# Kernel optimization log

Hardware: AMD Instinct MI355X
Metric: run time of the kernel (lower is better)

## Reference

```python
import jax, jax.numpy as jnp
import numpy as np

N, G, E = 100000, 32768, 1000000
F, H = 64, 64


def _mlp(x, w1, b1, w2, b2):
    # Linear -> SiLU -> Linear (matches nn.Sequential in the torch module)
    return jax.nn.silu(x @ w1 + b1) @ w2 + b2


def setup_inputs() -> dict:
    key = jax.random.key(0)
    ks = jax.random.split(key, 24)

    def lin(k, fan_in, fan_out):
        s = 1.0 / np.sqrt(fan_in)
        kw, kb = jax.random.split(k)
        w = jax.random.uniform(kw, (fan_in, fan_out), jnp.float32, -s, s)
        b = jax.random.uniform(kb, (fan_out,), jnp.float32, -s, s)
        return w, b

    node_w1, node_b1 = lin(ks[0], F, H)
    node_w2, node_b2 = lin(ks[1], H, H)
    edge_w1, edge_b1 = lin(ks[2], 6, H)
    edge_w2, edge_b2 = lin(ks[3], H, H)
    msg_w1, msg_b1 = lin(ks[4], 2 * H, H)
    msg_w2, msg_b2 = lin(ks[5], H, H)
    upd_w1, upd_b1 = lin(ks[6], H, H)
    upd_w2, upd_b2 = lin(ks[7], H, H)

    return {
        "node_features": jax.random.normal(ks[8], (N, F), jnp.float32),
        "node_pos": jax.random.normal(ks[9], (N, 3), jnp.float32),
        "grid_pos": jax.random.normal(ks[10], (G, 3), jnp.float32),
        "orientations": jax.random.normal(ks[11], (N, 3, 3), jnp.float32),
        "edge_index": jnp.stack([
            jax.random.randint(ks[12], (E,), 0, N),
            jax.random.randint(ks[13], (E,), 0, G),
        ]),
        "node_w1": node_w1, "node_b1": node_b1, "node_w2": node_w2, "node_b2": node_b2,
        "edge_w1": edge_w1, "edge_b1": edge_b1, "edge_w2": edge_w2, "edge_b2": edge_b2,
        "msg_w1": msg_w1, "msg_b1": msg_b1, "msg_w2": msg_w2, "msg_b2": msg_b2,
        "upd_w1": upd_w1, "upd_b1": upd_b1, "upd_w2": upd_w2, "upd_b2": upd_b2,
    }


def reference(node_features, node_pos, grid_pos, orientations, edge_index,
              node_w1, node_b1, node_w2, node_b2,
              edge_w1, edge_b1, edge_w2, edge_b2,
              msg_w1, msg_b1, msg_w2, msg_b2,
              upd_w1, upd_b1, upd_w2, upd_b2):
    source, target = edge_index[0], edge_index[1]
    num_grid = grid_pos.shape[0]

    # node MLP
    h_node = _mlp(node_features, node_w1, node_b1, node_w2, node_b2)  # [N,H]

    # per-edge message with orientation-aware projection
    pos_s = node_pos[source]                 # [E,3]
    rel = grid_pos[target] - pos_s           # [E,3]
    # bmm(rel[:,None,:], R[source]).squeeze(1) == einsum ei,eij->ej
    trel = jnp.einsum("ei,eij->ej", rel, orientations[source])
    edge_attr = jnp.concatenate([pos_s, trel], axis=-1)        # [E,6]
    e_feat = _mlp(edge_attr, edge_w1, edge_b1, edge_w2, edge_b2)
    msg_in = jnp.concatenate([h_node[source], e_feat], axis=-1)  # [E,2H]
    messages = _mlp(msg_in, msg_w1, msg_b1, msg_w2, msg_b2)      # [E,H]

    # scatter-mean into grid buckets (mask out-of-range targets)
    valid = (target >= 0) & (target < num_grid)
    idx = jnp.where(valid, target, 0)
    msg_masked = jnp.where(valid[:, None], messages, 0.0)
    sums = jax.ops.segment_sum(msg_masked, idx, num_segments=num_grid)
    cnts = jax.ops.segment_sum(valid.astype(jnp.float32), idx, num_segments=num_grid)
    grid_feat = sums / jnp.maximum(cnts, 1.0)[:, None]

    return _mlp(grid_feat, upd_w1, upd_b1, upd_w2, upd_b2)  # [G,H]
```

## Files before the change

### kernel.cpp

```cpp
#include <hip/hip_runtime.h>
#include <hip/hip_bf16.h>
#include <cstdint>

typedef __attribute__((ext_vector_type(8))) short short8;
typedef __attribute__((ext_vector_type(4))) float f32x4;
typedef unsigned short u16;

__device__ __forceinline__ float b2f(u16 u) {
  union { unsigned int i; float f; } v; v.i = ((unsigned int)u) << 16; return v.f;
}
__device__ __forceinline__ u16 f2b(float f) {
  __hip_bfloat16 h = __float2bfloat16(f);
  union { __hip_bfloat16 h; u16 u; } v; v.h = h; return v.u;
}
__device__ __forceinline__ float silu_f(float x) {
  return x * __builtin_amdgcn_rcpf(1.0f + __expf(-x));
}

__device__ __forceinline__ float loadF(const void* p, long i, int isf32) {
  if (isf32) return ((const float*)p)[i];
  return b2f(((const u16*)p)[i]);
}

__device__ __forceinline__ int sniffbit(u16 u) {
  unsigned e = (u >> 7) & 0xffu;
  return (e >= 0xC0u || (e < 0x40u && (u & 0x7fffu) != 0)) ? 1 : 0;
}

struct Ptrs { const void* p[20]; int n[20]; };

#define FW_EW1 0
#define FW_UW1 384
#define FW_UW2 4480
#define FW_UB1 8576
#define FW_UB2 8640
#define FW_EB1 8704
#define FW_EB2 8768
#define FW_MB1 8832
#define FW_MB2 8896
#define FW_TOTAL 8960

#define IMG_EW2 0
#define IMG_MW1 4608
#define IMG_MW2 13312
#define IMG_TOTAL 17920

#define PREP_BLOCKS 105
#define HIST_BLOCKS 1024

__global__ __launch_bounds__(256) void hist_detect_k(
    Ptrs a, const int* __restrict__ eidx, int* __restrict__ cnt8,
    int* __restrict__ flags, long E, int G)
{
  const int t = threadIdx.x;
  const int b = blockIdx.x;
  if (b < HIST_BLOCKS) {
    int* cs = cnt8 + (size_t)(b & 7) * G;
    long i = (long)b * 256 + t;
    const long stride = (long)HIST_BLOCKS * 256;
    for (; i < E; i += stride) {
      int tg = eidx[E + i];
      if (tg >= 0 && tg < G) atomicAdd(&cs[tg], 1);
    }
    return;
  }
  int j = b - HIST_BLOCKS;
  const u16* q = (const u16*)a.p[j];
  int n = a.n[j];
  int m = n < 4096 ? n : 4096;
  int cnt = 0;
  for (int i = t; i < m; i += 256) cnt += sniffbit(q[i]);
  __shared__ int tot;
  if (t == 0) tot = 0;
  __syncthreads();
  if (cnt) atomicAdd(&tot, cnt);
  __syncthreads();
  if (t == 0) flags[j] = (tot >= 2) ? 1 : 0;
}

__global__ __launch_bounds__(256) void scan_prep_node_k(
    Ptrs a, const int* __restrict__ flags,
    const int* __restrict__ cnt8, int* __restrict__ cursor8,
    int* __restrict__ bsum,
    u16* __restrict__ img, float* __restrict__ fw,
    u16* __restrict__ hout, int nrows, int G, int NB2)
{
  const int t = threadIdx.x;
  const int b = blockIdx.x;

  if (b < NB2) {
    __shared__ int sd[256];
    const long tot = 8L * G;
    long j0 = (long)b * 1024 + (long)t * 4;
    int v[4];
#pragma unroll
    for (int k = 0; k < 4; ++k) {
      long j = j0 + k;
      v[k] = (j < tot) ? cnt8[(size_t)(j & 7) * G + (j >> 3)] : 0;
    }
    int local = v[0] + v[1] + v[2] + v[3];
    sd[t] = local;
    __syncthreads();
    for (int off = 1; off < 256; off <<= 1) {
      int x2 = (t >= off) ? sd[t - off] : 0;
      __syncthreads();
      sd[t] += x2;
      __syncthreads();
    }
    int p = sd[t] - local;
#pragma unroll
    for (int k = 0; k < 4; ++k) {
      long j = j0 + k;
      if (j < tot) cursor8[(size_t)(j & 7) * G + (j >> 3)] = p;
      p += v[k];
    }
    if (t == 255) bsum[b] = sd[255];
    return;
  }

  if (b < NB2 + PREP_BLOCKS) {
    int i = (b - NB2) * 256 + t;
    if (i < IMG_TOTAL) {
      const void* bp; int fl; long si; bool real;
      if (i < IMG_MW1) { int nn = i / 72, k = i % 72; bp = a.p[10]; fl = flags[10]; real = k < 64; si = (long)k * 64 + nn; }
      else if (i < IMG_MW2) { int t2 = i - IMG_MW1; int nn = t2 / 136, k = t2 % 136; bp = a.p[12]; fl = flags[12]; real = k < 128; si = (long)k * 64 + nn; }
      else { int t2 = i - IMG_MW2; int nn = t2 / 72, k = t2 % 72; bp = a.p[14]; fl = flags[14]; real = k < 64; si = (long)k * 64 + nn; }
      u16 val = 0;
      if (real) val = f2b(loadF(bp, si, fl));
      img[i] = val;
    } else if (i < IMG_TOTAL + FW_TOTAL) {
      int j = i - IMG_TOTAL;
      const void* bp; int fl; long si;
      if (j < 384)        { bp = a.p[8];  fl = flags[8];  si = j; }
      else if (j < 4480)  { bp = a.p[16]; fl = flags[16]; si = j - 384; }
      else if (j < 8576)  { bp = a.p[18]; fl = flags[18]; si = j - 4480; }
      else {
        int bb = j - 8576; int seg = bb >> 6; si = bb & 63;
        switch (seg) {
          case 0: bp = a.p[17]; fl = flags[17]; break;
          case 1: bp = a.p[19]; fl = flags[19]; break;
          case 2: bp = a.p[9];  fl = flags[9];  break;
          case 3: bp = a.p[11]; fl = flags[11]; break;
          case 4: bp = a.p[13]; fl = flags[13]; break;
          default: bp = a.p[15]; fl = flags[15]; break;
        }
      }
      fw[j] = loadF(bp, si, fl);
    }
    return;
  }

  __shared__ float xs[64][68];
  __shared__ float w1s[64][68];
  __shared__ float w2s[64][68];
  __shared__ float b1s[64];
  __shared__ float b2s[64];
  const void* x = a.p[0];
  const int xf = flags[0], f1 = flags[4], fb1 = flags[5], f2 = flags[6], fb2 = flags[7];
  const long rbase = (long)(b - NB2 - PREP_BLOCKS) * 64;
  for (int i = t; i < 4096; i += 256) {
    int k = i >> 6, cc = i & 63;
    w1s[k][cc] = loadF(a.p[4], i, f1);
    w2s[k][cc] = loadF(a.p[6], i, f2);
  }
  if (t < 64) { b1s[t] = loadF(a.p[5], t, fb1); b2s[t] = loadF(a.p[7], t, fb2); }
  {
    int row = t >> 2, ch = t & 3;
    long rg = rbase + row;
    if (rg < nrows) {
      if (xf) {
        const float* xp = (const float*)x + rg * 64 + ch * 16;
#pragma unroll
        for (int m = 0; m < 16; ++m) xs[row][ch * 16 + m] = xp[m];
      } else {
        const u16* xp = (const u16*)x + rg * 64 + ch * 16;
#pragma unroll
        for (int m = 0; m < 16; ++m) xs[row][ch * 16 + m] = b2f(xp[m]);
      }
    } else {
#pragma unroll
      for (int m = 0; m < 16; ++m) xs[row][ch * 16 + m] = 0.f;
    }
  }
  __syncthreads();
  const int r0 = (t >> 4) * 4, c0 = (t & 15) * 4;
  float acc[4][4];
#pragma unroll
  for (int i = 0; i < 4; ++i)
#pragma unroll
    for (int j = 0; j < 4; ++j) acc[i][j] = b1s[c0 + j];
  for (int k = 0; k < 64; ++k) {
    float w0 = w1s[k][c0], w1v = w1s[k][c0 + 1], w2v = w1s[k][c0 + 2], w3v = w1s[k][c0 + 3];
#pragma unroll
    for (int i = 0; i < 4; ++i) {
      float av = xs[r0 + i][k];
      acc[i][0] = fmaf(av, w0, acc[i][0]);
      acc[i][1] = fmaf(av, w1v, acc[i][1]);
      acc[i][2] = fmaf(av, w2v, acc[i][2]);
      acc[i][3] = fmaf(av, w3v, acc[i][3]);
    }
  }
  __syncthreads();
#pragma unroll
  for (int i = 0; i < 4; ++i)
#pragma unroll
    for (int j = 0; j < 4; ++j) xs[r0 + i][c0 + j] = silu_f(acc[i][j]);
  __syncthreads();
  float acc2[4][4];
#pragma unroll
  for (int i = 0; i < 4; ++i)
#pragma unroll
    for (int j = 0; j < 4; ++j) acc2[i][j] = b2s[c0 + j];
  for (int k = 0; k < 64; ++k) {
    float w0 = w2s[k][c0], w1v = w2s[k][c0 + 1], w2v = w2s[k][c0 + 2], w3v = w2s[k][c0 + 3];
#pragma unroll
    for (int i = 0; i < 4; ++i) {
      float av = xs[r0 + i][k];
      acc2[i][0] = fmaf(av, w0, acc2[i][0]);
      acc2[i][1] = fmaf(av, w1v, acc2[i][1]);
      acc2[i][2] = fmaf(av, w2v, acc2[i][2]);
      acc2[i][3] = fmaf(av, w3v, acc2[i][3]);
    }
  }
#pragma unroll
  for (int i = 0; i < 4; ++i) {
    long rg = rbase + r0 + i;
    if (rg < nrows) {
#pragma unroll
      for (int j = 0; j < 4; ++j) hout[rg * 64 + c0 + j] = f2b(acc2[i][j]);
    }
  }
}

__global__ __launch_bounds__(256) void scat_k(const int* __restrict__ eidx,
                                              int* __restrict__ cursor8,
                                              const int* __restrict__ bsum,
                                              unsigned int* __restrict__ pkS,
                                              int* __restrict__ evp,
                                              long E, int G, int NB2) {
  __shared__ int bo[256];
  const int t = threadIdx.x;
  int v = (t < NB2) ? bsum[t] : 0;
  bo[t] = v;
  __syncthreads();
  for (int off = 1; off < 256; off <<= 1) {
    int x2 = (t >= off) ? bo[t - off] : 0;
    __syncthreads();
    bo[t] += x2;
    __syncthreads();
  }
  if (blockIdx.x == 0 && t == 0) *evp = bo[NB2 - 1];
  int excl = bo[t] - v;
  __syncthreads();
  bo[t] = excl;
  __syncthreads();
  const int c = blockIdx.x & 7;
  int* cur = cursor8 + (size_t)c * G;
  long i = (long)blockIdx.x * 256 + t;
  const long stride = (long)gridDim.x * 256;
  for (; i < E; i += stride) {
    int tg = eidx[E + i];
    if (tg >= 0 && tg < G) {
      int s = eidx[i];
      long j = ((long)tg << 3) | c;
      int p = atomicAdd(&cur[tg], 1) + bo[j >> 10];
      __builtin_nontemporal_store((unsigned int)s | ((unsigned int)tg << 17), pkS + p);
    }
  }
}

#define ETILES 4

__global__ __launch_bounds__(256, 5) void edge_kernel(
    const void* node_pos, const void* grid_pos, const void* orient,
    const unsigned int* __restrict__ pkS, const int* __restrict__ evp,
    const u16* __restrict__ h_node, const u16* __restrict__ img,
    const float* __restrict__ fw, const int* __restrict__ flags,
    float* __restrict__ sums, int G)
{
  __shared__ __align__(16) u16 pool[4][3328];
  __shared__ float eaf[64][6];
  __shared__ float w1e[6][64];
  __shared__ float biasE[4][64];
  __shared__ int tgt_s[64];

  const int t = threadIdx.x;
  const int pf = flags[1], gf = flags[2], of = flags[3];
  const int Ev = *evp;
  for (int i = t; i < 384; i += 256) w1e[i / 64][i % 64] = fw[FW_EW1 + i];
  { int seg = t >> 6, cc = t & 63; biasE[seg][cc] = fw[FW_EB1 + seg * 64 + cc]; }
  __syncthreads();

  const int lane = t & 63, w = t >> 6;
  const int q = lane >> 4, c = lane & 15;
  const int m0 = w * 16;
  u16 (* __restrict__ ef1w)[72] = (u16 (*)[72])&pool[w][0];
  u16 (* __restrict__ hAw)[136] = (u16 (*)[136])&pool[w][1152];
  float (* __restrict__ msgfw)[66] = (float (*)[66])&pool[w][1152];
  const u16* wE2 = img + IMG_EW2;
  const u16* wM1 = img + IMG_MW1;
  const u16* wM2 = img + IMG_MW2;
  const f32x4 z = {0.f, 0.f, 0.f, 0.f};

  const long blockBase = (long)blockIdx.x * (ETILES * 64);

  unsigned int pkt[ETILES];
#pragma unroll
  for (int tn = 0; tn < ETILES; ++tn) {
    long eg = blockBase + (long)tn * 64 + m0 + lane;
    pkt[tn] = (lane < 16 && eg < Ev) ? pkS[eg] : 0u;
  }

  float gps[3], ggp[3], gor[9];
  int gtg = -1;
  short8 hv0, hv1;

  auto prefetch = [&](int tn) {
    long tb = blockBase + (long)tn * 64;
    unsigned int pk = pkt[tn];
    int gs = (int)(pk & 0x1FFFFu);
    gtg = (int)(pk >> 17);
    if (tb + m0 + lane >= Ev) { gs = 0; gtg = -1; }
    if (lane < 16) {
      int tgc = (gtg >= 0) ? gtg : 0;
#pragma unroll
      for (int i = 0; i < 3; ++i) gps[i] = loadF(node_pos, (long)gs * 3 + i, pf);
#pragma unroll
      for (int i = 0; i < 3; ++i) ggp[i] = loadF(grid_pos, (long)tgc * 3 + i, gf);
#pragma unroll
      for (int i = 0; i < 9; ++i) gor[i] = loadF(orient, (long)gs * 9 + i, of);
    }
    unsigned int pk2 = (unsigned int)__shfl((int)pkt[tn], lane >> 2);
    int ss = ((tb + m0 + (lane >> 2)) < Ev) ? (int)(pk2 & 0x1FFFFu) : 0;
    const u16* hp = h_node + (long)ss * 64 + (lane & 3) * 16;
    hv0 = *(const short8*)hp;
    hv1 = *(const short8*)(hp + 8);
  };

  prefetch(0);

#pragma unroll
  for (int tile = 0; tile < ETILES; ++tile) {
    long base = blockBase + (long)tile * 64;
    if (base >= Ev) break;

    if (lane < 16) {
      tgt_s[m0 + lane] = gtg;
      float rel[3], tr[3];
#pragma unroll
      for (int i = 0; i < 3; ++i) rel[i] = ggp[i] - gps[i];
#pragma unroll
      for (int j = 0; j < 3; ++j) tr[j] = 0.f;
#pragma unroll
      for (int i = 0; i < 3; ++i)
#pragma unroll
        for (int j = 0; j < 3; ++j) tr[j] = fmaf(rel[i], gor[i * 3 + j], tr[j]);
      eaf[m0 + lane][0] = gps[0]; eaf[m0 + lane][1] = gps[1]; eaf[m0 + lane][2] = gps[2];
      eaf[m0 + lane][3] = tr[0]; eaf[m0 + lane][4] = tr[1]; eaf[m0 + lane][5] = tr[2];
    }
    {
      int er = lane >> 2, ch = lane & 3;
      *(short8*)&hAw[er][ch * 16] = hv0;
      *(short8*)&hAw[er][ch * 16 + 8] = hv1;
    }
    __syncthreads();

    {
      int e = lane >> 2, c0 = (lane & 3) * 16;
      int eb = m0 + e;
      float a0 = eaf[eb][0], a1 = eaf[eb][1], a2 = eaf[eb][2];
      float a3 = eaf[eb][3], a4 = eaf[eb][4], a5 = eaf[eb][5];
      __align__(16) u16 tmp[16];
#pragma unroll
      for (int j = 0; j < 16; ++j) {
        int cc = c0 + j;
        float acc = biasE[0][cc];
        acc = fmaf(a0, w1e[0][cc], acc);
        acc = fmaf(a1, w1e[1][cc], acc);
        acc = fmaf(a2, w1e[2][cc], acc);
        acc = fmaf(a3, w1e[3][cc], acc);
        acc = fmaf(a4, w1e[4][cc], acc);
        acc = fmaf(a5, w1e[5][cc], acc);
        tmp[j] = f2b(silu_f(acc));
      }
      *(short8*)&ef1w[e][c0] = *(const short8*)tmp;
      *(short8*)&ef1w[e][c0 + 8] = *(const short8*)(tmp + 8);
    }
    __builtin_amdgcn_wave_barrier();
    {
      short8 a0 = *(const short8*)&ef1w[c][q * 8];
      short8 a1 = *(const short8*)&ef1w[c][32 + q * 8];
#pragma unroll
      for (int nt = 0; nt < 4; ++nt) {
        short8 b0 = *(const short8*)&wE2[(nt * 16 + c) * 72 + q * 8];
        short8 b1v = *(const short8*)&wE2[(nt * 16 + c) * 72 + 32 + q * 8];
        f32x4 acc = __builtin_amdgcn_mfma_f32_16x16x32_bf16(a0, b0, z, 0, 0, 0);
        acc = __builtin_amdgcn_mfma_f32_16x16x32_bf16(a1, b1v, acc, 0, 0, 0);
#pragma unroll
        for (int r = 0; r < 4; ++r) {
          int row = q * 4 + r, col = nt * 16 + c;
          hAw[row][64 + col] = f2b(acc[r] + biasE[1][col]);
        }
      }
    }
    __builtin_amdgcn_wave_barrier();
    {
      short8 a0 = *(const short8*)&hAw[c][q * 8];
      short8 a1 = *(const short8*)&hAw[c][32 + q * 8];
      short8 a2 = *(const short8*)&hAw[c][64 + q * 8];
      short8 a3 = *(const short8*)&hAw[c][96 + q * 8];
#pragma unroll
      for (int nt = 0; nt < 4; ++nt) {
        const u16* wp = &wM1[(nt * 16 + c) * 136];
        f32x4 acc = __builtin_amdgcn_mfma_f32_16x16x32_bf16(a0, *(const short8*)(wp + q * 8), z, 0, 0, 0);
        acc = __builtin_amdgcn_mfma_f32_16x16x32_bf16(a1, *(const short8*)(wp + 32 + q * 8), acc, 0, 0, 0);
        acc = __builtin_amdgcn_mfma_f32_16x16x32_bf16(a2, *(const short8*)(wp + 64 + q * 8), acc, 0, 0, 0);
        acc = __builtin_amdgcn_mfma_f32_16x16x32_bf16(a3, *(const short8*)(wp + 96 + q * 8), acc, 0, 0, 0);
#pragma unroll
        for (int r = 0; r < 4; ++r) {
          int row = q * 4 + r, col = nt * 16 + c;
          ef1w[row][col] = f2b(silu_f(acc[r] + biasE[2][col]));
        }
      }
    }
    __builtin_amdgcn_wave_barrier();
    {
      short8 a0 = *(const short8*)&ef1w[c][q * 8];
      short8 a1 = *(const short8*)&ef1w[c][32 + q * 8];
      __builtin_amdgcn_wave_barrier();
#pragma unroll
      for (int nt = 0; nt < 4; ++nt) {
        short8 b0 = *(const short8*)&wM2[(nt * 16 + c) * 72 + q * 8];
        short8 b1v = *(const short8*)&wM2[(nt * 16 + c) * 72 + 32 + q * 8];
        f32x4 acc = __builtin_amdgcn_mfma_f32_16x16x32_bf16(a0, b0, z, 0, 0, 0);
        acc = __builtin_amdgcn_mfma_f32_16x16x32_bf16(a1, b1v, acc, 0, 0, 0);
#pragma unroll
        for (int r = 0; r < 4; ++r) {
          int row = q * 4 + r, col = nt * 16 + c;
          msgfw[row][col] = acc[r] + biasE[3][col];
        }
      }
    }
    __builtin_amdgcn_wave_barrier();

    __builtin_amdgcn_sched_barrier(0);
    if (tile + 1 < ETILES && base + 64 < Ev) prefetch(tile + 1);

    {
      int col = lane;
      int cur = tgt_s[m0];
      float run = msgfw[0][col];
      bool lopen = (m0 == 0) ? true : (tgt_s[m0 - 1] == cur);
#pragma unroll
      for (int r2 = 1; r2 < 16; ++r2) {
        int tg = tgt_s[m0 + r2];
        float v = msgfw[r2][col];
        if (tg == cur) {
          run += v;
        } else {
          if (cur >= 0) {
            if (lopen) unsafeAtomicAdd(&sums[(long)cur * 64 + col], run);
            else sums[(long)cur * 64 + col] = run;
          }
          cur = tg; run = v; lopen = false;
        }
      }
      bool ropen = (m0 + 16 >= 64) ? true : (tgt_s[m0 + 16] == cur);
      if (cur >= 0) {
        if (lopen || ropen) unsafeAtomicAdd(&sums[(long)cur * 64 + col], run);
        else sums[(long)cur * 64 + col] = run;
      }
    }
    __syncthreads();
  }
}

__global__ __launch_bounds__(256) void upd_mlp(
    const float* __restrict__ sums, const int* __restrict__ cnt8,
    const float* __restrict__ fw, float* __restrict__ out, int nrows)
{
  __shared__ float xs[64][68];
  __shared__ float w1s[64][68];
  __shared__ float w2s[64][68];
  __shared__ float b1s[64];
  __shared__ float b2s[64];
  const int t = threadIdx.x;
  const long rbase = (long)blockIdx.x * 64;
  for (int i = t; i < 4096; i += 256) {
    int k = i >> 6, cc = i & 63;
    w1s[k][cc] = fw[FW_UW1 + i];
    w2s[k][cc] = fw[FW_UW2 + i];
  }
  if (t < 64) { b1s[t] = fw[FW_UB1 + t]; b2s[t] = fw[FW_UB2 + t]; }
  {
    int row = t >> 2, ch = t & 3;
    long rg = rbase + row;
    if (rg < nrows) {
      int cn = 0;
#pragma unroll
      for (int cc = 0; cc < 8; ++cc) cn += cnt8[(size_t)cc * nrows + rg];
      float inv = 1.0f / fmaxf((float)cn, 1.0f);
      const float* p = sums + rg * 64 + ch * 16;
#pragma unroll
      for (int m = 0; m < 16; ++m) xs[row][ch * 16 + m] = p[m] * inv;
    } else {
#pragma unroll
      for (int m = 0; m < 16; ++m) xs[row][ch * 16 + m] = 0.f;
    }
  }
  __syncthreads();
  const int r0 = (t >> 4) * 4, c0 = (t & 15) * 4;
  float acc[4][4];
#pragma unroll
  for (int i = 0; i < 4; ++i)
#pragma unroll
    for (int j = 0; j < 4; ++j) acc[i][j] = b1s[c0 + j];
  for (int k = 0; k < 64; ++k) {
    float w0 = w1s[k][c0], w1v = w1s[k][c0 + 1], w2v = w1s[k][c0 + 2], w3v = w1s[k][c0 + 3];
#pragma unroll
    for (int i = 0; i < 4; ++i) {
      float av = xs[r0 + i][k];
      acc[i][0] = fmaf(av, w0, acc[i][0]);
      acc[i][1] = fmaf(av, w1v, acc[i][1]);
      acc[i][2] = fmaf(av, w2v, acc[i][2]);
      acc[i][3] = fmaf(av, w3v, acc[i][3]);
    }
  }
  __syncthreads();
#pragma unroll
  for (int i = 0; i < 4; ++i)
#pragma unroll
    for (int j = 0; j < 4; ++j) xs[r0 + i][c0 + j] = silu_f(acc[i][j]);
  __syncthreads();
  float acc2[4][4];
#pragma unroll
  for (int i = 0; i < 4; ++i)
#pragma unroll
    for (int j = 0; j < 4; ++j) acc2[i][j] = b2s[c0 + j];
  for (int k = 0; k < 64; ++k) {
    float w0 = w2s[k][c0], w1v = w2s[k][c0 + 1], w2v = w2s[k][c0 + 2], w3v = w2s[k][c0 + 3];
#pragma unroll
    for (int i = 0; i < 4; ++i) {
      float av = xs[r0 + i][k];
      acc2[i][0] = fmaf(av, w0, acc2[i][0]);
      acc2[i][1] = fmaf(av, w1v, acc2[i][1]);
      acc2[i][2] = fmaf(av, w2v, acc2[i][2]);
      acc2[i][3] = fmaf(av, w3v, acc2[i][3]);
    }
  }
#pragma unroll
  for (int i = 0; i < 4; ++i) {
    long rg = rbase + r0 + i;
    if (rg < nrows) {
#pragma unroll
      for (int j = 0; j < 4; ++j) out[rg * 64 + c0 + j] = acc2[i][j];
    }
  }
}

extern "C" void kernel_launch(void* const* d_in, const int* in_sizes, int n_in,
                              void* d_out, int out_size, void* d_ws, size_t ws_size,
                              hipStream_t stream) {
  const int N = in_sizes[1] / 3;
  const int G = in_sizes[2] / 3;
  const long E = (long)in_sizes[4] / 2;
  const int NB2 = (int)((8L * G + 1023) / 1024);
  const int nodeBlocks = (N + 63) / 64;

  char* ws = (char*)d_ws;
  float* sums = (float*)ws;
  size_t off = (size_t)G * 256;
  int* cnt8 = (int*)(ws + off);     off += (size_t)G * 32;
  int* cursor8 = (int*)(ws + off);  off += (size_t)G * 32;
  int* bsum = (int*)(ws + off);     off += 1024;
  int* evp = (int*)(ws + off);      off += 256;
  int* flags = (int*)(ws + off);    off += 256;
  unsigned int* pkS = (unsigned int*)(ws + off); off += (size_t)E * 4;
  u16* h_node = (u16*)(ws + off);   off += (size_t)N * 128;
  u16* img = (u16*)(ws + off);      off += (size_t)IMG_TOTAL * 2;
  float* fw = (float*)(ws + off);

  hipMemsetAsync(ws, 0, (size_t)G * 288, stream);

  Ptrs a;
  const int map[20] = {0,1,2,3, 5,6,7,8, 9,10,11,12, 13,14,15,16, 17,18,19,20};
  for (int i = 0; i < 20; ++i) { a.p[i] = d_in[map[i]]; a.n[i] = in_sizes[map[i]]; }

  hist_detect_k<<<HIST_BLOCKS + 20, 256, 0, stream>>>(
      a, (const int*)d_in[4], cnt8, flags, E, G);
  scan_prep_node_k<<<NB2 + PREP_BLOCKS + nodeBlocks, 256, 0, stream>>>(
      a, flags, cnt8, cursor8, bsum, img, fw, h_node, N, G, NB2);
  scat_k<<<1024, 256, 0, stream>>>((const int*)d_in[4], cursor8, bsum, pkS, evp, E, G, NB2);
  edge_kernel<<<(int)((E + ETILES * 64 - 1) / (ETILES * 64)), 256, 0, stream>>>(
      d_in[1], d_in[2], d_in[3], pkS, evp, h_node, img, fw, flags, sums, G);
  upd_mlp<<<(G + 63) / 64, 256, 0, stream>>>(sums, cnt8, fw, (float*)d_out, G);
}
```

Before: 512.2 us.

## Double-buffer edge targets and cut block barriers in edge kernel

Makes the shared target array double-buffered and writes each tile's targets during the prefetch step. This lets the mid-tile block-wide __syncthreads be replaced by a wave barrier, leaving one raw s_barrier per tile. The geometry prefetch becomes a macro with scalarized registers and packed indices held in rotating scalars, which is meant to avoid dynamic register-array indexing. The risk is correctness, because the segment-run logic reads other waves' target entries across wave boundaries.

```diff
diff --git a/kernel.cpp b/kernel.cpp
--- a/kernel.cpp
+++ b/kernel.cpp
@@ -282,14 +282,13 @@
   __shared__ float eaf[64][6];
   __shared__ float w1e[6][64];
   __shared__ float biasE[4][64];
-  __shared__ int tgt_s[64];
+  __shared__ int tgt_s[2][64];
 
   const int t = threadIdx.x;
   const int pf = flags[1], gf = flags[2], of = flags[3];
   const int Ev = *evp;
   for (int i = t; i < 384; i += 256) w1e[i / 64][i % 64] = fw[FW_EW1 + i];
   { int seg = t >> 6, cc = t & 63; biasE[seg][cc] = fw[FW_EB1 + seg * 64 + cc]; }
-  __syncthreads();
 
   const int lane = t & 63, w = t >> 6;
   const int q = lane >> 4, c = lane & 15;
@@ -304,66 +303,71 @@
 
   const long blockBase = (long)blockIdx.x * (ETILES * 64);
 
-  unsigned int pkt[ETILES];
-#pragma unroll
-  for (int tn = 0; tn < ETILES; ++tn) {
-    long eg = blockBase + (long)tn * 64 + m0 + lane;
-    pkt[tn] = (lane < 16 && eg < Ev) ? pkS[eg] : 0u;
-  }
-
-  float gps[3], ggp[3], gor[9];
-  int gtg = -1;
+  unsigned int pkA = 0, pkB = 0, pkC = 0, pkD = 0;
+  if (lane < 16) {
+    long e0 = blockBase + m0 + lane;
+    if (e0 < Ev)       pkA = pkS[e0];
+    if (e0 + 64 < Ev)  pkB = pkS[e0 + 64];
+    if (e0 + 128 < Ev) pkC = pkS[e0 + 128];
+    if (e0 + 192 < Ev) pkD = pkS[e0 + 192];
+  }
+
+  float gps0, gps1, gps2, ggp0, ggp1, ggp2;
+  float gor0, gor1, gor2, gor3, gor4, gor5, gor6, gor7, gor8;
   short8 hv0, hv1;
 
-  auto prefetch = [&](int tn) {
-    long tb = blockBase + (long)tn * 64;
-    unsigned int pk = pkt[tn];
-    int gs = (int)(pk & 0x1FFFFu);
-    gtg = (int)(pk >> 17);
-    if (tb + m0 + lane >= Ev) { gs = 0; gtg = -1; }
-    if (lane < 16) {
-      int tgc = (gtg >= 0) ? gtg : 0;
-#pragma unroll
-      for (int i = 0; i < 3; ++i) gps[i] = loadF(node_pos, (long)gs * 3 + i, pf);
-#pragma unroll
-      for (int i = 0; i < 3; ++i) ggp[i] = loadF(grid_pos, (long)tgc * 3 + i, gf);
-#pragma unroll
-      for (int i = 0; i < 9; ++i) gor[i] = loadF(orient, (long)gs * 9 + i, of);
-    }
-    unsigned int pk2 = (unsigned int)__shfl((int)pkt[tn], lane >> 2);
-    int ss = ((tb + m0 + (lane >> 2)) < Ev) ? (int)(pk2 & 0x1FFFFu) : 0;
-    const u16* hp = h_node + (long)ss * 64 + (lane & 3) * 16;
-    hv0 = *(const short8*)hp;
-    hv1 = *(const short8*)(hp + 8);
-  };
-
-  prefetch(0);
-
-#pragma unroll
+#define GEO_PREFETCH(TB, PKV, TSLOT) do {                                    \
+    unsigned int pku_ = (PKV);                                               \
+    int gs_ = (int)(pku_ & 0x1FFFFu);                                        \
+    int gtg_ = (int)(pku_ >> 17);                                            \
+    if ((TB) + m0 + lane >= Ev) { gs_ = 0; gtg_ = -1; }                      \
+    if (lane < 16) {                                                         \
+      tgt_s[TSLOT][m0 + lane] = gtg_;                                        \
+      int tgc_ = (gtg_ >= 0) ? gtg_ : 0;                                     \
+      gps0 = loadF(node_pos, (long)gs_ * 3 + 0, pf);                         \
+      gps1 = loadF(node_pos, (long)gs_ * 3 + 1, pf);                         \
+      gps2 = loadF(node_pos, (long)gs_ * 3 + 2, pf);                         \
+      ggp0 = loadF(grid_pos, (long)tgc_ * 3 + 0, gf);                        \
+      ggp1 = loadF(grid_pos, (long)tgc_ * 3 + 1, gf);                        \
+      ggp2 = loadF(grid_pos, (long)tgc_ * 3 + 2, gf);                        \
+      gor0 = loadF(orient, (long)gs_ * 9 + 0, of);                           \
+      gor1 = loadF(orient, (long)gs_ * 9 + 1, of);                           \
+      gor2 = loadF(orient, (long)gs_ * 9 + 2, of);                           \
+      gor3 = loadF(orient, (long)gs_ * 9 + 3, of);                           \
+      gor4 = loadF(orient, (long)gs_ * 9 + 4, of);                           \
+      gor5 = loadF(orient, (long)gs_ * 9 + 5, of);                           \
+      gor6 = loadF(orient, (long)gs_ * 9 + 6, of);                           \
+      gor7 = loadF(orient, (long)gs_ * 9 + 7, of);                           \
+    }                                                                        \
+    gor8 = (lane < 16) ? loadF(orient, (long)gs_ * 9 + 8, of) : 0.f;         \
+    unsigned int pks_ = (unsigned int)__shfl((int)(PKV), lane >> 2);         \
+    int ss_ = (((TB) + m0 + (lane >> 2)) < Ev) ? (int)(pks_ & 0x1FFFFu) : 0; \
+    const u16* hp_ = h_node + (long)ss_ * 64 + (lane & 3) * 16;              \
+    hv0 = *(const short8*)hp_;                                               \
+    hv1 = *(const short8*)(hp_ + 8);                                         \
+  } while (0)
+
+  GEO_PREFETCH(blockBase, pkA, 0);
+  __syncthreads();
+
   for (int tile = 0; tile < ETILES; ++tile) {
     long base = blockBase + (long)tile * 64;
     if (base >= Ev) break;
 
     if (lane < 16) {
-      tgt_s[m0 + lane] = gtg;
-      float rel[3], tr[3];
-#pragma unroll
-      for (int i = 0; i < 3; ++i) rel[i] = ggp[i] - gps[i];
-#pragma unroll
-      for (int j = 0; j < 3; ++j) tr[j] = 0.f;
-#pragma unroll
-      for (int i = 0; i < 3; ++i)
-#pragma unroll
-        for (int j = 0; j < 3; ++j) tr[j] = fmaf(rel[i], gor[i * 3 + j], tr[j]);
-      eaf[m0 + lane][0] = gps[0]; eaf[m0 + lane][1] = gps[1]; eaf[m0 + lane][2] = gps[2];
-      eaf[m0 + lane][3] = tr[0]; eaf[m0 + lane][4] = tr[1]; eaf[m0 + lane][5] = tr[2];
+      float rel0 = ggp0 - gps0, rel1 = ggp1 - gps1, rel2 = ggp2 - gps2;
+      float tr0 = rel0 * gor0; tr0 = fmaf(rel1, gor3, tr0); tr0 = fmaf(rel2, gor6, tr0);
+      float tr1 = rel0 * gor1; tr1 = fmaf(rel1, gor4, tr1); tr1 = fmaf(rel2, gor7, tr1);
+      float tr2 = rel0 * gor2; tr2 = fmaf(rel1, gor5, tr2); tr2 = fmaf(rel2, gor8, tr2);
+      eaf[m0 + lane][0] = gps0; eaf[m0 + lane][1] = gps1; eaf[m0 + lane][2] = gps2;
+      eaf[m0 + lane][3] = tr0;  eaf[m0 + lane][4] = tr1;  eaf[m0 + lane][5] = tr2;
     }
     {
       int er = lane >> 2, ch = lane & 3;
       *(short8*)&hAw[er][ch * 16] = hv0;
       *(short8*)&hAw[er][ch * 16 + 8] = hv1;
     }
-    __syncthreads();
+    __builtin_amdgcn_wave_barrier();
 
     {
       int e = lane >> 2, c0 = (lane & 3) * 16;
@@ -444,16 +448,20 @@
     __builtin_amdgcn_wave_barrier();
 
     __builtin_amdgcn_sched_barrier(0);
-    if (tile + 1 < ETILES && base + 64 < Ev) prefetch(tile + 1);
+    if (tile + 1 < ETILES && base + 64 < Ev) {
+      unsigned int pkn = pkB; pkB = pkC; pkC = pkD;
+      GEO_PREFETCH(base + 64, pkn, (tile + 1) & 1);
+    }
 
     {
+      const int* tg_ = tgt_s[tile & 1];
       int col = lane;
-      int cur = tgt_s[m0];
+      int cur = tg_[m0];
       float run = msgfw[0][col];
-      bool lopen = (m0 == 0) ? true : (tgt_s[m0 - 1] == cur);
+      bool lopen = (m0 == 0) ? true : (tg_[m0 - 1] == cur);
 #pragma unroll
       for (int r2 = 1; r2 < 16; ++r2) {
-        int tg = tgt_s[m0 + r2];
+        int tg = tg_[m0 + r2];
         float v = msgfw[r2][col];
         if (tg == cur) {
           run += v;
@@ -465,14 +473,18 @@
           cur = tg; run = v; lopen = false;
         }
       }
-      bool ropen = (m0 + 16 >= 64) ? true : (tgt_s[m0 + 16] == cur);
+      bool ropen = (m0 + 16 >= 64) ? true : (tg_[m0 + 16] == cur);
       if (cur >= 0) {
         if (lopen || ropen) unsafeAtomicAdd(&sums[(long)cur * 64 + col], run);
         else sums[(long)cur * 64 + col] = run;
       }
     }
-    __syncthreads();
-  }
+    __builtin_amdgcn_wave_barrier();
+
+    asm volatile("s_waitcnt lgkmcnt(0)" ::: "memory");
+    __builtin_amdgcn_s_barrier();
+  }
+#undef GEO_PREFETCH
 }
 
 __global__ __launch_bounds__(256) void upd_mlp(
```

Measured after the change: 551.1 us. 7.6% more time.
